# Kernel tuning notes

Measured on AMD Instinct MI355X. Metric: run time of the kernel, lower is better.

The kernel has to match this reference:

```python
import jax, jax.numpy as jnp
import numpy as np

B, I, O, S, C = 64, 2048, 2048, 10, 512  # batch, input, output, dendritic segments, context dim


def setup_inputs() -> dict:
    key = jax.random.key(0)
    ks = jax.random.split(key, 8)
    x = jax.random.normal(ks[0], (B, I), dtype=jnp.float32)
    context = jax.random.normal(ks[1], (B, C), dtype=jnp.float32)
    prev_activation = jax.random.normal(ks[2], (B, I), dtype=jnp.float32)
    # sparse-initialized weight: randn/sqrt(I) * (rand > sparsity)
    w = jax.random.normal(ks[3], (O, I), dtype=jnp.float32) / np.sqrt(I)
    mask = (jax.random.uniform(ks[4], (O, I)) > 0.9).astype(jnp.float32)
    weight = w * mask
    bias = jnp.zeros((O,), dtype=jnp.float32)
    astrocyte_activation = jnp.ones((O,), dtype=jnp.float32)
    astrocyte_threshold = jnp.full((O,), 0.5, dtype=jnp.float32)
    dendrite_segments = jax.random.normal(ks[5], (O, I, S), dtype=jnp.float32) / np.sqrt(I)
    dendritic_gates = jnp.ones((O, S), dtype=jnp.float32)
    connection_strength = jnp.ones((O, I), dtype=jnp.float32)
    pruning_threshold = jnp.full((1,), 0.01, dtype=jnp.float32)
    return {
        "x": x, "context": context, "prev_activation": prev_activation,
        "weight": weight, "bias": bias,
        "astrocyte_activation": astrocyte_activation,
        "astrocyte_threshold": astrocyte_threshold,
        "dendrite_segments": dendrite_segments,
        "dendritic_gates": dendritic_gates,
        "connection_strength": connection_strength,
        "pruning_threshold": pruning_threshold,
    }


def reference(x, context, prev_activation, weight, bias, astrocyte_activation,
              astrocyte_threshold, dendrite_segments, dendritic_gates,
              connection_strength, pruning_threshold):
    dt = x.dtype
    # structural plasticity (eval branch): prune weak connections
    conn_mask = (jnp.abs(weight) * connection_strength > pruning_threshold[0]).astype(dt)
    eff_w = weight * conn_mask  # [O, I]
    # astrocyte modulation
    ctx_signal = jnp.mean(context, axis=-1, keepdims=True)          # [B, 1]
    astro = jax.nn.sigmoid(ctx_signal * astrocyte_activation[None, :])  # [B, O]
    astro = astro * (astro > astrocyte_threshold[None, :]).astype(dt)
    mean_astro = jnp.mean(astro, axis=0)                            # [O]
    mod_w = eff_w * mean_astro[:, None]                             # [O, I]
    synaptic = x @ mod_w.T + bias                                   # [B, O]
    # multi-compartment dendritic processing
    seg_act = jnp.einsum('bi,ois->bos', x, dendrite_segments)       # [B, O, S]
    gated = jax.nn.relu(seg_act) * jax.nn.sigmoid(dendritic_gates)[None, :, :]
    dendritic = jnp.sum(gated, axis=-1)                             # [B, O]
    return jax.nn.relu(synaptic + dendritic)
```

## Files before the change

### kernel.cpp

```cpp
#include <hip/hip_runtime.h>
#include <math.h>

#define Bn 64
#define In 2048
#define On 2048
#define Sn 10
#define Cn 512

#define KT 64
#define NT (In / KT)
#define LROW 72
#define NR 16

typedef short short8 __attribute__((ext_vector_type(8)));
typedef float f32x4 __attribute__((ext_vector_type(4)));

__device__ __forceinline__ unsigned short f2bf(float f) {
    union { float f; unsigned u; } v; v.f = f;
    unsigned r = (v.u + 0x7FFFu + ((v.u >> 16) & 1u)) >> 16;
    return (unsigned short)r;
}
__device__ __forceinline__ float sigmoidf_(float x) { return 1.0f / (1.0f + expf(-x)); }

__global__ void prep_kernel(const float* __restrict__ x,
                            const float* __restrict__ ctx,
                            float* __restrict__ ws_ctx,
                            unsigned short* __restrict__ ws_xbf) {
    const int b = blockIdx.x;
    const int t = threadIdx.x;
    if (b < Bn) {
        __shared__ float red[256];
        float s = ctx[b * Cn + t] + ctx[b * Cn + t + 256];
        red[t] = s;
        __syncthreads();
        for (int off = 128; off > 0; off >>= 1) {
            if (t < off) red[t] += red[t + off];
            __syncthreads();
        }
        if (t == 0) ws_ctx[b] = red[0] * (1.0f / (float)Cn);
    } else {
        int idx = (b - Bn) * 256 + t;
        ws_xbf[idx] = f2bf(x[idx]);
    }
}

__global__ __launch_bounds__(64, 2)
void main_kernel(const unsigned short* __restrict__ xbf,
                 const float* __restrict__ wgt,
                 const float* __restrict__ cst,
                 const float* __restrict__ seg,
                 const float* __restrict__ bias,
                 const float* __restrict__ aact,
                 const float* __restrict__ athr,
                 const float* __restrict__ gates,
                 const float* __restrict__ prn,
                 const float* __restrict__ ws_ctx,
                 float* __restrict__ out) {
    __shared__ __align__(16) unsigned short Blds[2][NR * LROW];

    const int lane = threadIdx.x;
    const int o = blockIdx.x;
    const int l15 = lane & 15;
    const int q = lane >> 4;
    const float pthr = prn[0];

    for (int idx = lane; idx < 5 * LROW; idx += 64) {
        Blds[0][11 * LROW + idx] = 0;
        Blds[1][11 * LROW + idx] = 0;
    }

    const float aa = aact[o], th = athr[o];
    float sg = sigmoidf_(ws_ctx[lane] * aa);
    float ma = (sg > th) ? sg : 0.0f;
#pragma unroll
    for (int m = 32; m; m >>= 1) ma += __shfl_xor(ma, m, 64);
    const float mastro = ma * (1.0f / (float)Bn);

    const float gsig = (l15 < 10) ? sigmoidf_(gates[o * Sn + l15]) : 0.0f;

    int sego[5], ldso[5];
#pragma unroll
    for (int j = 0; j < 5; ++j) {
        const int f = lane + 64 * j;
        const int io = f / 5;
        const int s2 = (f - io * 5) * 2;
        sego[j] = io * Sn + s2;
        ldso[j] = s2 * LROW + io;
    }
    const float* segbase = seg + (size_t)o * In * Sn;
    const float* wrow = wgt + (size_t)o * In;
    const float* crow = cst + (size_t)o * In;
    const unsigned short* xrow = xbf + (size_t)l15 * In + q * 8;

    float2 SA[5], SB[5];
    float wA, cA, wB, cB;
    short8 AA[4][2], AB[4][2];

    f32x4 acc[4];
#pragma unroll
    for (int mt = 0; mt < 4; ++mt) acc[mt] = (f32x4){0.f, 0.f, 0.f, 0.f};

    auto loadSeg = [&](float2 (&S)[5], float& w, float& c, int t) {
        const float* p = segbase + t * (KT * Sn);
#pragma unroll
        for (int j = 0; j < 5; ++j) S[j] = *(const float2*)(p + sego[j]);
        w = wrow[t * KT + lane];
        c = crow[t * KT + lane];
    };
    auto loadA = [&](short8 (&A)[4][2], int t) {
#pragma unroll
        for (int mt = 0; mt < 4; ++mt) {
            const unsigned short* p = xrow + (size_t)mt * 16 * In + t * KT;
            A[mt][0] = *(const short8*)(p);
            A[mt][1] = *(const short8*)(p + 32);
        }
    };
    auto storeT = [&](float2 (&S)[5], float w, float c, int bb) {
        unsigned short* B = Blds[bb];
#pragma unroll
        for (int j = 0; j < 5; ++j) {
            B[ldso[j]] = f2bf(S[j].x);
            B[ldso[j] + LROW] = f2bf(S[j].y);
        }
        const float e = (__builtin_fabsf(w) * c > pthr) ? w : 0.0f;
        B[10 * LROW + lane] = f2bf(e);
    };
    auto computeT = [&](short8 (&A)[4][2], int bb) {
        const unsigned short* Bp = &Blds[bb][l15 * LROW + q * 8];
        short8 b0 = *(const short8*)(Bp);
        short8 b1 = *(const short8*)(Bp + 32);
#pragma unroll
        for (int mt = 0; mt < 4; ++mt) {
            acc[mt] = __builtin_amdgcn_mfma_f32_16x16x32_bf16(A[mt][0], b0, acc[mt], 0, 0, 0);
            acc[mt] = __builtin_amdgcn_mfma_f32_16x16x32_bf16(A[mt][1], b1, acc[mt], 0, 0, 0);
        }
    };

    loadSeg(SA, wA, cA, 0);
    loadSeg(SB, wB, cB, 1);
    loadA(AA, 0);
    storeT(SA, wA, cA, 0);
    for (int u = 0; u < NT / 2; ++u) {
        const int t = 2 * u;
        const int tp1 = (t + 1 < NT) ? t + 1 : NT - 1;
        const int tp2 = (t + 2 < NT) ? t + 2 : NT - 1;
        const int tp3 = (t + 3 < NT) ? t + 3 : NT - 1;
        loadSeg(SA, wA, cA, tp2);
        loadA(AB, tp1);
        computeT(AA, 0);
        storeT(SB, wB, cB, 1);
        loadSeg(SB, wB, cB, tp3);
        loadA(AA, tp2);
        computeT(AB, 1);
        storeT(SA, wA, cA, 0);
    }

    const float bo = bias[o];
#pragma unroll
    for (int mt = 0; mt < 4; ++mt) {
#pragma unroll
        for (int r = 0; r < 4; ++r) {
            const float v = acc[mt][r];
            float contrib;
            if (l15 < 10)       contrib = (v > 0.f ? v : 0.f) * gsig;
            else if (l15 == 10) contrib = mastro * v;
            else                contrib = 0.f;
            contrib += __shfl_xor(contrib, 1, 64);
            contrib += __shfl_xor(contrib, 2, 64);
            contrib += __shfl_xor(contrib, 4, 64);
            contrib += __shfl_xor(contrib, 8, 64);
            if (l15 == 0) {
                const int b = mt * 16 + q * 4 + r;
                const float ov = contrib + bo;
                out[(size_t)b * On + o] = ov > 0.f ? ov : 0.f;
            }
        }
    }
}

extern "C" void kernel_launch(void* const* d_in, const int* in_sizes, int n_in,
                              void* d_out, int out_size, void* d_ws, size_t ws_size,
                              hipStream_t stream) {
    (void)in_sizes; (void)n_in; (void)out_size; (void)ws_size;
    const float* x    = (const float*)d_in[0];
    const float* ctx  = (const float*)d_in[1];
    const float* wgt  = (const float*)d_in[3];
    const float* bias = (const float*)d_in[4];
    const float* aact = (const float*)d_in[5];
    const float* athr = (const float*)d_in[6];
    const float* seg  = (const float*)d_in[7];
    const float* gat  = (const float*)d_in[8];
    const float* cst  = (const float*)d_in[9];
    const float* prn  = (const float*)d_in[10];
    float* out = (float*)d_out;

    float* ws_ctx = (float*)d_ws;
    unsigned short* ws_xbf = (unsigned short*)((char*)d_ws + 256);

    prep_kernel<<<Bn + (Bn * In) / 256, 256, 0, stream>>>(x, ctx, ws_ctx, ws_xbf);
    main_kernel<<<On, 64, 0, stream>>>(ws_xbf, wgt, cst, seg, bias, aact,
                                       athr, gat, prn, ws_ctx, out);
}
```

Baseline: 298.5 us.

## Replace bf16 MFMA path with FP32 packed FMA per batch lane

Drops the bf16 MFMA tiling and LDS transpose. Each block now has each lane own one batch row and accumulate the ten segment dot products plus the synaptic dot product with packed FP32 FMAs. The prep kernel now writes a transposed x and a precomputed pruned weight matrix, so the main loop reads the segment tensor with wave-uniform vector loads and no per-tile conversion or synchronisation. The cost is far more arithmetic without tensor cores, extra prep traffic for the pruned weights, and low parallelism per block over a large streamed tensor.

```diff
diff --git a/kernel.cpp b/kernel.cpp
--- a/kernel.cpp
+++ b/kernel.cpp
@@ -7,25 +7,20 @@
 #define Sn 10
 #define Cn 512
 
-#define KT 64
-#define NT (In / KT)
-#define LROW 72
-#define NR 16
+typedef float f32x4 __attribute__((ext_vector_type(4)));
+typedef float f32x2 __attribute__((ext_vector_type(2)));
 
-typedef short short8 __attribute__((ext_vector_type(8)));
-typedef float f32x4 __attribute__((ext_vector_type(4)));
-
-__device__ __forceinline__ unsigned short f2bf(float f) {
-    union { float f; unsigned u; } v; v.f = f;
-    unsigned r = (v.u + 0x7FFFu + ((v.u >> 16) & 1u)) >> 16;
-    return (unsigned short)r;
-}
 __device__ __forceinline__ float sigmoidf_(float x) { return 1.0f / (1.0f + expf(-x)); }
 
-__global__ void prep_kernel(const float* __restrict__ x,
-                            const float* __restrict__ ctx,
-                            float* __restrict__ ws_ctx,
-                            unsigned short* __restrict__ ws_xbf) {
+__global__ __launch_bounds__(256)
+void prep_kernel(const float* __restrict__ x,
+                 const float* __restrict__ ctx,
+                 const float* __restrict__ wgt,
+                 const float* __restrict__ cst,
+                 const float* __restrict__ prn,
+                 float* __restrict__ ws_ctx,
+                 float* __restrict__ xT,
+                 float* __restrict__ effw) {
     const int b = blockIdx.x;
     const int t = threadIdx.x;
     if (b < Bn) {
@@ -38,36 +33,56 @@
             __syncthreads();
         }
         if (t == 0) ws_ctx[b] = red[0] * (1.0f / (float)Cn);
+    } else if (b < Bn + 32) {
+        __shared__ float T[64][65];
+        const int i0 = (b - Bn) * 64;
+        const int row = t >> 4;
+        const int col4 = (t & 15) * 4;
+#pragma unroll
+        for (int r = 0; r < 4; ++r) {
+            const int rr = row + r * 16;
+            f32x4 v = *(const f32x4*)(x + (size_t)rr * In + i0 + col4);
+            T[col4 + 0][rr] = v[0];
+            T[col4 + 1][rr] = v[1];
+            T[col4 + 2][rr] = v[2];
+            T[col4 + 3][rr] = v[3];
+        }
+        __syncthreads();
+        const int il = t >> 2;
+        const int c = (t & 3) * 16;
+        float* dst = xT + (size_t)(i0 + il) * Bn + c;
+#pragma unroll
+        for (int k = 0; k < 16; k += 4)
+            *(f32x4*)(dst + k) = *(const f32x4*)(&T[il][c + k]);
     } else {
-        int idx = (b - Bn) * 256 + t;
-        ws_xbf[idx] = f2bf(x[idx]);
+        const float thr = prn[0];
+        const size_t base = (size_t)(b - Bn - 32) * 8192;
+#pragma unroll
+        for (int k = 0; k < 8; ++k) {
+            const size_t idx = base + ((size_t)k * 256 + t) * 4;
+            f32x4 w = *(const f32x4*)(wgt + idx);
+            f32x4 c4 = *(const f32x4*)(cst + idx);
+            f32x4 e;
+#pragma unroll
+            for (int j = 0; j < 4; ++j)
+                e[j] = (__builtin_fabsf(w[j]) * c4[j] > thr) ? w[j] : 0.0f;
+            *(f32x4*)(effw + idx) = e;
+        }
     }
 }
 
-__global__ __launch_bounds__(64, 2)
-void main_kernel(const unsigned short* __restrict__ xbf,
-                 const float* __restrict__ wgt,
-                 const float* __restrict__ cst,
+__global__ __launch_bounds__(64, 4)
+void main_kernel(const float* __restrict__ xT,
+                 const float* __restrict__ effw,
                  const float* __restrict__ seg,
                  const float* __restrict__ bias,
                  const float* __restrict__ aact,
                  const float* __restrict__ athr,
                  const float* __restrict__ gates,
-                 const float* __restrict__ prn,
                  const float* __restrict__ ws_ctx,
                  float* __restrict__ out) {
-    __shared__ __align__(16) unsigned short Blds[2][NR * LROW];
-
     const int lane = threadIdx.x;
     const int o = blockIdx.x;
-    const int l15 = lane & 15;
-    const int q = lane >> 4;
-    const float pthr = prn[0];
-
-    for (int idx = lane; idx < 5 * LROW; idx += 64) {
-        Blds[0][11 * LROW + idx] = 0;
-        Blds[1][11 * LROW + idx] = 0;
-    }
 
     const float aa = aact[o], th = athr[o];
     float sg = sigmoidf_(ws_ctx[lane] * aa);
@@ -76,106 +91,78 @@
     for (int m = 32; m; m >>= 1) ma += __shfl_xor(ma, m, 64);
     const float mastro = ma * (1.0f / (float)Bn);
 
-    const float gsig = (l15 < 10) ? sigmoidf_(gates[o * Sn + l15]) : 0.0f;
+    const float* sp = seg + (size_t)o * In * Sn;
+    const float* ep = effw + (size_t)o * In;
+    const float* xp = xT + lane;
 
-    int sego[5], ldso[5];
+    f32x2 acc2[5];
 #pragma unroll
-    for (int j = 0; j < 5; ++j) {
-        const int f = lane + 64 * j;
-        const int io = f / 5;
-        const int s2 = (f - io * 5) * 2;
-        sego[j] = io * Sn + s2;
-        ldso[j] = s2 * LROW + io;
-    }
-    const float* segbase = seg + (size_t)o * In * Sn;
-    const float* wrow = wgt + (size_t)o * In;
-    const float* crow = cst + (size_t)o * In;
-    const unsigned short* xrow = xbf + (size_t)l15 * In + q * 8;
+    for (int k = 0; k < 5; ++k) acc2[k] = (f32x2){0.f, 0.f};
+    float asyn = 0.0f;
 
-    float2 SA[5], SB[5];
-    float wA, cA, wB, cB;
-    short8 AA[4][2], AB[4][2];
+#pragma unroll 4
+    for (int g = 0; g < In / 4; ++g) {
+        const float* s4 = sp + g * 40;
+        f32x4 q0 = *(const f32x4*)(s4 + 0);
+        f32x4 q1 = *(const f32x4*)(s4 + 4);
+        f32x4 q2 = *(const f32x4*)(s4 + 8);
+        f32x4 q3 = *(const f32x4*)(s4 + 12);
+        f32x4 q4 = *(const f32x4*)(s4 + 16);
+        f32x4 q5 = *(const f32x4*)(s4 + 20);
+        f32x4 q6 = *(const f32x4*)(s4 + 24);
+        f32x4 q7 = *(const f32x4*)(s4 + 28);
+        f32x4 q8 = *(const f32x4*)(s4 + 32);
+        f32x4 q9 = *(const f32x4*)(s4 + 36);
+        f32x4 ew = *(const f32x4*)(ep + g * 4);
+        const float x0 = xp[(size_t)(g * 4 + 0) * Bn];
+        const float x1 = xp[(size_t)(g * 4 + 1) * Bn];
+        const float x2 = xp[(size_t)(g * 4 + 2) * Bn];
+        const float x3 = xp[(size_t)(g * 4 + 3) * Bn];
 
-    f32x4 acc[4];
-#pragma unroll
-    for (int mt = 0; mt < 4; ++mt) acc[mt] = (f32x4){0.f, 0.f, 0.f, 0.f};
+        f32x2 xx;
+        xx = (f32x2){x0, x0};
+        acc2[0] += xx * (f32x2){q0[0], q0[1]};
+        acc2[1] += xx * (f32x2){q0[2], q0[3]};
+        acc2[2] += xx * (f32x2){q1[0], q1[1]};
+        acc2[3] += xx * (f32x2){q1[2], q1[3]};
+        acc2[4] += xx * (f32x2){q2[0], q2[1]};
+        xx = (f32x2){x1, x1};
+        acc2[0] += xx * (f32x2){q2[2], q2[3]};
+        acc2[1] += xx * (f32x2){q3[0], q3[1]};
+        acc2[2] += xx * (f32x2){q3[2], q3[3]};
+        acc2[3] += xx * (f32x2){q4[0], q4[1]};
+        acc2[4] += xx * (f32x2){q4[2], q4[3]};
+        xx = (f32x2){x2, x2};
+        acc2[0] += xx * (f32x2){q5[0], q5[1]};
+        acc2[1] += xx * (f32x2){q5[2], q5[3]};
+        acc2[2] += xx * (f32x2){q6[0], q6[1]};
+        acc2[3] += xx * (f32x2){q6[2], q6[3]};
+        acc2[4] += xx * (f32x2){q7[0], q7[1]};
+        xx = (f32x2){x3, x3};
+        acc2[0] += xx * (f32x2){q7[2], q7[3]};
+        acc2[1] += xx * (f32x2){q8[0], q8[1]};
+        acc2[2] += xx * (f32x2){q8[2], q8[3]};
+        acc2[3] += xx * (f32x2){q9[0], q9[1]};
+        acc2[4] += xx * (f32x2){q9[2], q9[3]};
 
-    auto loadSeg = [&](float2 (&S)[5], float& w, float& c, int t) {
-        const float* p = segbase + t * (KT * Sn);
-#pragma unroll
-        for (int j = 0; j < 5; ++j) S[j] = *(const float2*)(p + sego[j]);
-        w = wrow[t * KT + lane];
-        c = crow[t * KT + lane];
-    };
-    auto loadA = [&](short8 (&A)[4][2], int t) {
-#pragma unroll
-        for (int mt = 0; mt < 4; ++mt) {
-            const unsigned short* p = xrow + (size_t)mt * 16 * In + t * KT;
-            A[mt][0] = *(const short8*)(p);
-            A[mt][1] = *(const short8*)(p + 32);
-        }
-    };
-    auto storeT = [&](float2 (&S)[5], float w, float c, int bb) {
-        unsigned short* B = Blds[bb];
-#pragma unroll
-        for (int j = 0; j < 5; ++j) {
-            B[ldso[j]] = f2bf(S[j].x);
-            B[ldso[j] + LROW] = f2bf(S[j].y);
-        }
-        const float e = (__builtin_fabsf(w) * c > pthr) ? w : 0.0f;
-        B[10 * LROW + lane] = f2bf(e);
-    };
-    auto computeT = [&](short8 (&A)[4][2], int bb) {
-        const unsigned short* Bp = &Blds[bb][l15 * LROW + q * 8];
-        short8 b0 = *(const short8*)(Bp);
-        short8 b1 = *(const short8*)(Bp + 32);
-#pragma unroll
-        for (int mt = 0; mt < 4; ++mt) {
-            acc[mt] = __builtin_amdgcn_mfma_f32_16x16x32_bf16(A[mt][0], b0, acc[mt], 0, 0, 0);
-            acc[mt] = __builtin_amdgcn_mfma_f32_16x16x32_bf16(A[mt][1], b1, acc[mt], 0, 0, 0);
-        }
-    };
-
-    loadSeg(SA, wA, cA, 0);
-    loadSeg(SB, wB, cB, 1);
-    loadA(AA, 0);
-    storeT(SA, wA, cA, 0);
-    for (int u = 0; u < NT / 2; ++u) {
-        const int t = 2 * u;
-        const int tp1 = (t + 1 < NT) ? t + 1 : NT - 1;
-        const int tp2 = (t + 2 < NT) ? t + 2 : NT - 1;
-        const int tp3 = (t + 3 < NT) ? t + 3 : NT - 1;
-        loadSeg(SA, wA, cA, tp2);
-        loadA(AB, tp1);
-        computeT(AA, 0);
-        storeT(SB, wB, cB, 1);
-        loadSeg(SB, wB, cB, tp3);
-        loadA(AA, tp2);
-        computeT(AB, 1);
-        storeT(SA, wA, cA, 0);
+        asyn = fmaf(ew[0], x0, asyn);
+        asyn = fmaf(ew[1], x1, asyn);
+        asyn = fmaf(ew[2], x2, asyn);
+        asyn = fmaf(ew[3], x3, asyn);
     }
 
-    const float bo = bias[o];
+    float dend = 0.0f;
 #pragma unroll
-    for (int mt = 0; mt < 4; ++mt) {
+    for (int s2 = 0; s2 < 5; ++s2) {
 #pragma unroll
-        for (int r = 0; r < 4; ++r) {
-            const float v = acc[mt][r];
-            float contrib;
-            if (l15 < 10)       contrib = (v > 0.f ? v : 0.f) * gsig;
-            else if (l15 == 10) contrib = mastro * v;
-            else                contrib = 0.f;
-            contrib += __shfl_xor(contrib, 1, 64);
-            contrib += __shfl_xor(contrib, 2, 64);
-            contrib += __shfl_xor(contrib, 4, 64);
-            contrib += __shfl_xor(contrib, 8, 64);
-            if (l15 == 0) {
-                const int b = mt * 16 + q * 4 + r;
-                const float ov = contrib + bo;
-                out[(size_t)b * On + o] = ov > 0.f ? ov : 0.f;
-            }
+        for (int h = 0; h < 2; ++h) {
+            float v = acc2[s2][h];
+            v = v > 0.0f ? v : 0.0f;
+            dend += v * sigmoidf_(gates[o * Sn + s2 * 2 + h]);
         }
     }
+    const float r = dend + mastro * asyn + bias[o];
+    out[(size_t)lane * On + o] = r > 0.0f ? r : 0.0f;
 }
 
 extern "C" void kernel_launch(void* const* d_in, const int* in_sizes, int n_in,
@@ -195,9 +182,11 @@
     float* out = (float*)d_out;
 
     float* ws_ctx = (float*)d_ws;
-    unsigned short* ws_xbf = (unsigned short*)((char*)d_ws + 256);
+    float* xT     = (float*)((char*)d_ws + 256);
+    float* effw   = (float*)((char*)d_ws + 256 + In * Bn * 4);
 
-    prep_kernel<<<Bn + (Bn * In) / 256, 256, 0, stream>>>(x, ctx, ws_ctx, ws_xbf);
-    main_kernel<<<On, 64, 0, stream>>>(ws_xbf, wgt, cst, seg, bias, aact,
-                                       athr, gat, prn, ws_ctx, out);
+    prep_kernel<<<Bn + 32 + 512, 256, 0, stream>>>(x, ctx, wgt, cst, prn,
+                                                   ws_ctx, xT, effw);
+    main_kernel<<<On, 64, 0, stream>>>(xT, effw, seg, bias, aact, athr,
+                                       gat, ws_ctx, out);
 }
```

Result: slower. 577.1 us (+93.3%).

## Deepen segment prefetch to four tiles with macro-unrolled scalar registers

Applied to the files above, without the earlier changes.

Replaces the lambda/array-based double-buffered loop with explicit macro-expanded scalar registers and four in-flight segment-load buffers, so global loads for dendrite segments run up to four tiles ahead of compute. It also drops the clamped tile indices and peels the tail explicitly. The aim is to hide more HBM latency in this bandwidth-bound streaming kernel and to avoid register arrays being spilled to scratch. The cost is higher VGPR pressure, which may threaten the two-waves launch bound occupancy.

```diff
diff --git a/kernel.cpp b/kernel.cpp
--- a/kernel.cpp
+++ b/kernel.cpp
@@ -44,6 +44,53 @@
     }
 }
 
+#define LOADSEG(N, tile) do {                                                  \
+    const float* p_ = segbase + (size_t)(tile) * (KT * Sn);                    \
+    s##N##_0 = *(const float2*)(p_ + so0);                                     \
+    s##N##_1 = *(const float2*)(p_ + so1);                                     \
+    s##N##_2 = *(const float2*)(p_ + so2);                                     \
+    s##N##_3 = *(const float2*)(p_ + so3);                                     \
+    s##N##_4 = *(const float2*)(p_ + so4);                                     \
+    w##N = wrow[(tile) * KT + lane];                                           \
+    c##N = crow[(tile) * KT + lane];                                           \
+} while (0)
+
+#define LOADA(P, tile) do {                                                    \
+    const unsigned short* p_ = xrow + (tile) * KT;                             \
+    a##P##_00 = *(const short8*)(p_);                                          \
+    a##P##_01 = *(const short8*)(p_ + 32);                                     \
+    a##P##_10 = *(const short8*)(p_ + 16 * In);                                \
+    a##P##_11 = *(const short8*)(p_ + 16 * In + 32);                           \
+    a##P##_20 = *(const short8*)(p_ + 32 * In);                                \
+    a##P##_21 = *(const short8*)(p_ + 32 * In + 32);                           \
+    a##P##_30 = *(const short8*)(p_ + 48 * In);                                \
+    a##P##_31 = *(const short8*)(p_ + 48 * In + 32);                           \
+} while (0)
+
+#define STOREB(N, Bl) do {                                                     \
+    Bl[lo0] = f2bf(s##N##_0.x);  Bl[lo0 + LROW] = f2bf(s##N##_0.y);            \
+    Bl[lo1] = f2bf(s##N##_1.x);  Bl[lo1 + LROW] = f2bf(s##N##_1.y);            \
+    Bl[lo2] = f2bf(s##N##_2.x);  Bl[lo2 + LROW] = f2bf(s##N##_2.y);            \
+    Bl[lo3] = f2bf(s##N##_3.x);  Bl[lo3 + LROW] = f2bf(s##N##_3.y);            \
+    Bl[lo4] = f2bf(s##N##_4.x);  Bl[lo4 + LROW] = f2bf(s##N##_4.y);            \
+    const float e_ = (__builtin_fabsf(w##N) * c##N > pthr) ? w##N : 0.0f;      \
+    Bl[10 * LROW + lane] = f2bf(e_);                                           \
+} while (0)
+
+#define COMPUTE(Bl, P) do {                                                    \
+    const unsigned short* Bp_ = &Bl[l15 * LROW + q * 8];                       \
+    short8 b0_ = *(const short8*)(Bp_);                                        \
+    short8 b1_ = *(const short8*)(Bp_ + 32);                                   \
+    acc0 = __builtin_amdgcn_mfma_f32_16x16x32_bf16(a##P##_00, b0_, acc0, 0, 0, 0); \
+    acc0 = __builtin_amdgcn_mfma_f32_16x16x32_bf16(a##P##_01, b1_, acc0, 0, 0, 0); \
+    acc1 = __builtin_amdgcn_mfma_f32_16x16x32_bf16(a##P##_10, b0_, acc1, 0, 0, 0); \
+    acc1 = __builtin_amdgcn_mfma_f32_16x16x32_bf16(a##P##_11, b1_, acc1, 0, 0, 0); \
+    acc2 = __builtin_amdgcn_mfma_f32_16x16x32_bf16(a##P##_20, b0_, acc2, 0, 0, 0); \
+    acc2 = __builtin_amdgcn_mfma_f32_16x16x32_bf16(a##P##_21, b1_, acc2, 0, 0, 0); \
+    acc3 = __builtin_amdgcn_mfma_f32_16x16x32_bf16(a##P##_30, b0_, acc3, 0, 0, 0); \
+    acc3 = __builtin_amdgcn_mfma_f32_16x16x32_bf16(a##P##_31, b1_, acc3, 0, 0, 0); \
+} while (0)
+
 __global__ __launch_bounds__(64, 2)
 void main_kernel(const unsigned short* __restrict__ xbf,
                  const float* __restrict__ wgt,
@@ -56,7 +103,8 @@
                  const float* __restrict__ prn,
                  const float* __restrict__ ws_ctx,
                  float* __restrict__ out) {
-    __shared__ __align__(16) unsigned short Blds[2][NR * LROW];
+    __shared__ __align__(16) unsigned short Blds0[NR * LROW];
+    __shared__ __align__(16) unsigned short Blds1[NR * LROW];
 
     const int lane = threadIdx.x;
     const int o = blockIdx.x;
@@ -65,117 +113,84 @@
     const float pthr = prn[0];
 
     for (int idx = lane; idx < 5 * LROW; idx += 64) {
-        Blds[0][11 * LROW + idx] = 0;
-        Blds[1][11 * LROW + idx] = 0;
+        Blds0[11 * LROW + idx] = 0;
+        Blds1[11 * LROW + idx] = 0;
     }
 
     const float aa = aact[o], th = athr[o];
-    float sg = sigmoidf_(ws_ctx[lane] * aa);
-    float ma = (sg > th) ? sg : 0.0f;
+    float sgv = sigmoidf_(ws_ctx[lane] * aa);
+    float ma = (sgv > th) ? sgv : 0.0f;
 #pragma unroll
     for (int m = 32; m; m >>= 1) ma += __shfl_xor(ma, m, 64);
     const float mastro = ma * (1.0f / (float)Bn);
 
     const float gsig = (l15 < 10) ? sigmoidf_(gates[o * Sn + l15]) : 0.0f;
 
-    int sego[5], ldso[5];
-#pragma unroll
-    for (int j = 0; j < 5; ++j) {
-        const int f = lane + 64 * j;
-        const int io = f / 5;
-        const int s2 = (f - io * 5) * 2;
-        sego[j] = io * Sn + s2;
-        ldso[j] = s2 * LROW + io;
+    int so0, so1, so2, so3, so4, lo0, lo1, lo2, lo3, lo4;
+    {
+        int f, io, s2;
+        f = lane;       io = f / 5; s2 = (f - io * 5) * 2; so0 = io * Sn + s2; lo0 = s2 * LROW + io;
+        f = lane + 64;  io = f / 5; s2 = (f - io * 5) * 2; so1 = io * Sn + s2; lo1 = s2 * LROW + io;
+        f = lane + 128; io = f / 5; s2 = (f - io * 5) * 2; so2 = io * Sn + s2; lo2 = s2 * LROW + io;
+        f = lane + 192; io = f / 5; s2 = (f - io * 5) * 2; so3 = io * Sn + s2; lo3 = s2 * LROW + io;
+        f = lane + 256; io = f / 5; s2 = (f - io * 5) * 2; so4 = io * Sn + s2; lo4 = s2 * LROW + io;
     }
     const float* segbase = seg + (size_t)o * In * Sn;
     const float* wrow = wgt + (size_t)o * In;
     const float* crow = cst + (size_t)o * In;
     const unsigned short* xrow = xbf + (size_t)l15 * In + q * 8;
 
-    float2 SA[5], SB[5];
-    float wA, cA, wB, cB;
-    short8 AA[4][2], AB[4][2];
-
-    f32x4 acc[4];
-#pragma unroll
-    for (int mt = 0; mt < 4; ++mt) acc[mt] = (f32x4){0.f, 0.f, 0.f, 0.f};
-
-    auto loadSeg = [&](float2 (&S)[5], float& w, float& c, int t) {
-        const float* p = segbase + t * (KT * Sn);
-#pragma unroll
-        for (int j = 0; j < 5; ++j) S[j] = *(const float2*)(p + sego[j]);
-        w = wrow[t * KT + lane];
-        c = crow[t * KT + lane];
-    };
-    auto loadA = [&](short8 (&A)[4][2], int t) {
-#pragma unroll
-        for (int mt = 0; mt < 4; ++mt) {
-            const unsigned short* p = xrow + (size_t)mt * 16 * In + t * KT;
-            A[mt][0] = *(const short8*)(p);
-            A[mt][1] = *(const short8*)(p + 32);
-        }
-    };
-    auto storeT = [&](float2 (&S)[5], float w, float c, int bb) {
-        unsigned short* B = Blds[bb];
-#pragma unroll
-        for (int j = 0; j < 5; ++j) {
-            B[ldso[j]] = f2bf(S[j].x);
-            B[ldso[j] + LROW] = f2bf(S[j].y);
-        }
-        const float e = (__builtin_fabsf(w) * c > pthr) ? w : 0.0f;
-        B[10 * LROW + lane] = f2bf(e);
-    };
-    auto computeT = [&](short8 (&A)[4][2], int bb) {
-        const unsigned short* Bp = &Blds[bb][l15 * LROW + q * 8];
-        short8 b0 = *(const short8*)(Bp);
-        short8 b1 = *(const short8*)(Bp + 32);
-#pragma unroll
-        for (int mt = 0; mt < 4; ++mt) {
-            acc[mt] = __builtin_amdgcn_mfma_f32_16x16x32_bf16(A[mt][0], b0, acc[mt], 0, 0, 0);
-            acc[mt] = __builtin_amdgcn_mfma_f32_16x16x32_bf16(A[mt][1], b1, acc[mt], 0, 0, 0);
-        }
-    };
-
-    loadSeg(SA, wA, cA, 0);
-    loadSeg(SB, wB, cB, 1);
-    loadA(AA, 0);
-    storeT(SA, wA, cA, 0);
-    for (int u = 0; u < NT / 2; ++u) {
-        const int t = 2 * u;
-        const int tp1 = (t + 1 < NT) ? t + 1 : NT - 1;
-        const int tp2 = (t + 2 < NT) ? t + 2 : NT - 1;
-        const int tp3 = (t + 3 < NT) ? t + 3 : NT - 1;
-        loadSeg(SA, wA, cA, tp2);
-        loadA(AB, tp1);
-        computeT(AA, 0);
-        storeT(SB, wB, cB, 1);
-        loadSeg(SB, wB, cB, tp3);
-        loadA(AA, tp2);
-        computeT(AB, 1);
-        storeT(SA, wA, cA, 0);
-    }
+    float2 sA_0, sA_1, sA_2, sA_3, sA_4; float wA, cA;
+    float2 sB_0, sB_1, sB_2, sB_3, sB_4; float wB, cB;
+    float2 sC_0, sC_1, sC_2, sC_3, sC_4; float wC, cC;
+    float2 sD_0, sD_1, sD_2, sD_3, sD_4; float wD, cD;
+    short8 aE_00, aE_01, aE_10, aE_11, aE_20, aE_21, aE_30, aE_31;
+    short8 aO_00, aO_01, aO_10, aO_11, aO_20, aO_21, aO_30, aO_31;
+
+    f32x4 acc0 = (f32x4){0.f, 0.f, 0.f, 0.f};
+    f32x4 acc1 = (f32x4){0.f, 0.f, 0.f, 0.f};
+    f32x4 acc2 = (f32x4){0.f, 0.f, 0.f, 0.f};
+    f32x4 acc3 = (f32x4){0.f, 0.f, 0.f, 0.f};
+
+    LOADSEG(A, 0); LOADSEG(B, 1); LOADSEG(C, 2); LOADSEG(D, 3);
+    LOADA(E, 0);
+    STOREB(A, Blds0); STOREB(B, Blds1);
+
+    for (int u = 0; u < 7; ++u) {
+        const int t4 = u * 4;
+        LOADA(O, t4 + 1); LOADSEG(A, t4 + 4); COMPUTE(Blds0, E); STOREB(C, Blds0);
+        LOADA(E, t4 + 2); LOADSEG(B, t4 + 5); COMPUTE(Blds1, O); STOREB(D, Blds1);
+        LOADA(O, t4 + 3); LOADSEG(C, t4 + 6); COMPUTE(Blds0, E); STOREB(A, Blds0);
+        LOADA(E, t4 + 4); LOADSEG(D, t4 + 7); COMPUTE(Blds1, O); STOREB(B, Blds1);
+    }
+
+    LOADA(O, 29); COMPUTE(Blds0, E); STOREB(C, Blds0);
+    LOADA(E, 30); COMPUTE(Blds1, O); STOREB(D, Blds1);
+    LOADA(O, 31); COMPUTE(Blds0, E);
+    COMPUTE(Blds1, O);
 
     const float bo = bias[o];
-#pragma unroll
-    for (int mt = 0; mt < 4; ++mt) {
-#pragma unroll
-        for (int r = 0; r < 4; ++r) {
-            const float v = acc[mt][r];
-            float contrib;
-            if (l15 < 10)       contrib = (v > 0.f ? v : 0.f) * gsig;
-            else if (l15 == 10) contrib = mastro * v;
-            else                contrib = 0.f;
-            contrib += __shfl_xor(contrib, 1, 64);
-            contrib += __shfl_xor(contrib, 2, 64);
-            contrib += __shfl_xor(contrib, 4, 64);
-            contrib += __shfl_xor(contrib, 8, 64);
-            if (l15 == 0) {
-                const int b = mt * 16 + q * 4 + r;
-                const float ov = contrib + bo;
-                out[(size_t)b * On + o] = ov > 0.f ? ov : 0.f;
-            }
-        }
-    }
+#define EPI(accv, mt) do {                                                     \
+    _Pragma("unroll")                                                          \
+    for (int r = 0; r < 4; ++r) {                                              \
+        const float v = accv[r];                                               \
+        float contrib;                                                         \
+        if (l15 < 10)       contrib = (v > 0.f ? v : 0.f) * gsig;              \
+        else if (l15 == 10) contrib = mastro * v;                              \
+        else                contrib = 0.f;                                     \
+        contrib += __shfl_xor(contrib, 1, 64);                                 \
+        contrib += __shfl_xor(contrib, 2, 64);                                 \
+        contrib += __shfl_xor(contrib, 4, 64);                                 \
+        contrib += __shfl_xor(contrib, 8, 64);                                 \
+        if (l15 == 0) {                                                        \
+            const int b_ = (mt) * 16 + q * 4 + r;                              \
+            const float ov = contrib + bo;                                     \
+            out[(size_t)b_ * On + o] = ov > 0.f ? ov : 0.f;                    \
+        }                                                                      \
+    }                                                                          \
+} while (0)
+    EPI(acc0, 0); EPI(acc1, 1); EPI(acc2, 2); EPI(acc3, 3);
+#undef EPI
 }
 
 extern "C" void kernel_launch(void* const* d_in, const int* in_sizes, int n_in,
```

New measurement: 301.4 us. Within noise of the previous version (+0.9%).
